# Optimization experiments

Measured on AMD Instinct MI355X. Metric: run time of the kernel, lower is better.

Reference implementation:

```python
import jax, jax.numpy as jnp
from jax import lax
import numpy as np

P, K1, K2 = 8, 5, 9  # nPaths, small/large ECA kernel sizes (from nDim=1024, nPaths=8)
LN_EPS = 1e-5


def setup_inputs() -> dict:
    key = jax.random.key(0)
    ks = jax.random.split(key, 6)
    b, c, l = 16, 1024, 4096
    return {
        "x": jax.random.normal(ks[0], (b, c, l), dtype=jnp.float32),
        "conv1_w": jax.random.normal(ks[1], (P, K1), dtype=jnp.float32) * 0.3,
        "conv2_w": jax.random.normal(ks[2], (P, K2), dtype=jnp.float32) * 0.3,
        "combine_w": jax.random.normal(ks[3], (2,), dtype=jnp.float32) * 0.5,
        "combine_b": jnp.zeros((), dtype=jnp.float32),
        "ln_g": jnp.ones((P,), dtype=jnp.float32),
        "ln_b": jnp.zeros((P,), dtype=jnp.float32),
        "W1": jax.random.normal(ks[4], (P, 2 * P), dtype=jnp.float32) * 0.3,
        "b1": jnp.zeros((2 * P,), dtype=jnp.float32),
        "W2": jax.random.normal(ks[5], (2 * P, P), dtype=jnp.float32) * 0.3,
        "b2": jnp.zeros((P,), dtype=jnp.float32),
    }


def _grouped_conv(y, w):
    # y: (b, P, D) pooled per-path features; w: (P, k) one 1-ch kernel per path.
    # Equivalent to the per-path Conv1d(1,1,k, padding=(k-1)//2) loop, fused.
    k = w.shape[-1]
    pad = (k - 1) // 2
    return lax.conv_general_dilated(
        y, w[:, None, :], window_strides=(1,), padding=[(pad, pad)],
        dimension_numbers=("NCH", "OIH", "NCH"), feature_group_count=y.shape[1])


def reference(x, conv1_w, conv2_w, combine_w, combine_b, ln_g, ln_b, W1, b1, W2, b2):
    b, c, l = x.shape
    nP = conv1_w.shape[0]
    D = c // nP
    pf = x.reshape(b, nP, D, l)          # (b, P, D, l)
    y = pf.mean(-1)                      # (b, P, D) global-avg-pool over l
    y1 = _grouped_conv(y, conv1_w)       # (b, P, D)
    y2 = _grouped_conv(y, conv2_w)       # (b, P, D)
    # combine = Conv1d(2,1,1): scalar mix of the two conv outputs + bias
    attn = jax.nn.sigmoid(combine_w[0] * y1 + combine_w[1] * y2 + combine_b)
    # cross-path gating MLP on per-path mean attention
    cross = attn.mean(-1)                # (b, P)
    mu = cross.mean(-1, keepdims=True)
    var = cross.var(-1, keepdims=True)   # biased, matches torch LayerNorm
    h = (cross - mu) / jnp.sqrt(var + LN_EPS) * ln_g + ln_b
    h = jax.nn.gelu(h @ W1 + b1, approximate=False)
    gate = jax.nn.sigmoid(h @ W2 + b2)   # (b, P)
    scale = attn * gate[:, :, None]      # (b, P, D)
    out = pf * scale[..., None]          # broadcast over l
    return out.reshape(b, c, l)
```

## Files before the change

kernel.cpp:

```cpp
#include <hip/hip_runtime.h>
#include <math.h>

#define NP 8
#define ND 128
#define NC 1024
#define NL 4096
#define NB 16
#define LN_EPS 1e-5f

#define NBLK 2048
#define NCHUNK 4
#define RPC 2
#define GRPS 64

typedef float v4f __attribute__((ext_vector_type(4)));

__device__ __forceinline__ float hsum(v4f v) { return v.x + v.y + v.z + v.w; }
__device__ __forceinline__ float sigmoid_f(float z) { return 1.f / (1.f + expf(-z)); }

__device__ __forceinline__ float gelu_f(float s) {
    const float t = 0.7978845608028654f * (s + 0.044715f * s * s * s);
    const float e = expf(2.f * t);
    return 0.5f * s * (1.f + (e - 1.f) / (e + 1.f));
}

__global__ __launch_bounds__(256, 8) void fused_kernel(
    const float* __restrict__ x, float* __restrict__ y,
    unsigned* __restrict__ garr, unsigned* __restrict__ grel,
    unsigned* __restrict__ root,
    const float* __restrict__ conv1_w, const float* __restrict__ conv2_w,
    const float* __restrict__ combine_w, const float* __restrict__ combine_b,
    const float* __restrict__ ln_g, const float* __restrict__ ln_b,
    const float* __restrict__ W1, const float* __restrict__ b1,
    const float* __restrict__ W2, const float* __restrict__ b2,
    float* __restrict__ out)
{
    const int tid    = threadIdx.x;
    const int bid    = blockIdx.x;
    const int grp    = bid >> 5;
    const bool lead  = (bid & 31) == 0;

    __shared__ float sred[RPC][4];
    __shared__ float sy[NC];
    __shared__ float sattn[NC];
    __shared__ float scross[NP];
    __shared__ float sh[NP];
    __shared__ float sh2[2 * NP];
    __shared__ float sgate[NP];
    __shared__ float sml[2];

    for (int c = 0; c < NCHUNK; ++c) {
        const int r0  = c * (NBLK * RPC) + RPC * bid;
        const int b   = r0 >> 10;
        const int ch0 = r0 & (NC - 1);
        const v4f* x0 = (const v4f*)x + (size_t)r0 * (NL / 4);
        v4f* o0       = (v4f*)out    + (size_t)r0 * (NL / 4);

        #pragma unroll
        for (int r = 0; r < RPC; ++r) {
            const v4f* xr = x0 + (size_t)r * (NL / 4);
            float ps = hsum(xr[tid]) + hsum(xr[tid + 256])
                     + hsum(xr[tid + 512]) + hsum(xr[tid + 768]);
            ps += __shfl_down(ps, 32, 64); ps += __shfl_down(ps, 16, 64);
            ps += __shfl_down(ps, 8, 64);  ps += __shfl_down(ps, 4, 64);
            ps += __shfl_down(ps, 2, 64);  ps += __shfl_down(ps, 1, 64);
            if ((tid & 63) == 0) sred[r][tid >> 6] = ps;
        }
        __syncthreads();
        if (tid == 0) {
            #pragma unroll
            for (int r = 0; r < RPC; ++r) {
                const float ym = (sred[r][0] + sred[r][1] + sred[r][2] + sred[r][3]) * (1.f / NL);
                __hip_atomic_store(&y[r0 + r], ym, __ATOMIC_RELAXED, __HIP_MEMORY_SCOPE_AGENT);
            }
            unsigned old = __hip_atomic_fetch_add(&garr[grp], 1u,
                              __ATOMIC_RELEASE, __HIP_MEMORY_SCOPE_AGENT);
            if (old == (unsigned)(c * 32 + 31))
                __hip_atomic_fetch_add(root, 1u,
                              __ATOMIC_RELEASE, __HIP_MEMORY_SCOPE_AGENT);
            if (lead) {
                while (__hip_atomic_load(root, __ATOMIC_RELAXED,
                                         __HIP_MEMORY_SCOPE_AGENT) < (unsigned)((c + 1) * GRPS))
                    __builtin_amdgcn_s_sleep(4);
                __hip_atomic_store(&grel[grp], (unsigned)(c + 1),
                                   __ATOMIC_RELAXED, __HIP_MEMORY_SCOPE_AGENT);
            } else {
                while (__hip_atomic_load(&grel[grp], __ATOMIC_RELAXED,
                                         __HIP_MEMORY_SCOPE_AGENT) < (unsigned)(c + 1))
                    __builtin_amdgcn_s_sleep(4);
            }
        }
        __syncthreads();

        const float* yb = y + b * NC;
        #pragma unroll
        for (int k = 0; k < 4; ++k) {
            const int i = tid + 256 * k;
            sy[i] = __hip_atomic_load(&yb[i], __ATOMIC_RELAXED, __HIP_MEMORY_SCOPE_AGENT);
        }
        __syncthreads();
        #pragma unroll
        for (int k = 0; k < 4; ++k) {
            const int pos = tid + 256 * k;
            const int p = pos >> 7, d = pos & 127;
            const float* rowp = sy + p * ND;
            float c1 = 0.f;
            #pragma unroll
            for (int t = 0; t < 5; ++t) {
                int dd = d + t - 2;
                float v = (dd >= 0 && dd < ND) ? rowp[dd] : 0.f;
                c1 += conv1_w[p * 5 + t] * v;
            }
            float c2 = 0.f;
            #pragma unroll
            for (int t = 0; t < 9; ++t) {
                int dd = d + t - 4;
                float v = (dd >= 0 && dd < ND) ? rowp[dd] : 0.f;
                c2 += conv2_w[p * 9 + t] * v;
            }
            sattn[pos] = sigmoid_f(combine_w[0] * c1 + combine_w[1] * c2 + combine_b[0]);
        }
        __syncthreads();
        if (tid < 128) {
            const int p = tid >> 4, o = (tid & 15) * 8;
            float s = 0.f;
            #pragma unroll
            for (int j = 0; j < 8; ++j) s += sattn[p * ND + o + j];
            s += __shfl_down(s, 8, 16); s += __shfl_down(s, 4, 16);
            s += __shfl_down(s, 2, 16); s += __shfl_down(s, 1, 16);
            if ((tid & 15) == 0) scross[p] = s * (1.f / ND);
        }
        __syncthreads();
        if (tid == 0) {
            float mu = 0.f;
            #pragma unroll
            for (int pp = 0; pp < NP; ++pp) mu += scross[pp];
            mu *= (1.f / NP);
            float var = 0.f;
            #pragma unroll
            for (int pp = 0; pp < NP; ++pp) { float dl = scross[pp] - mu; var += dl * dl; }
            sml[0] = mu;
            sml[1] = rsqrtf(var * (1.f / NP) + LN_EPS);
        }
        __syncthreads();
        if (tid < NP)
            sh[tid] = (scross[tid] - sml[0]) * sml[1] * ln_g[tid] + ln_b[tid];
        __syncthreads();
        if (tid < 2 * NP) {
            float s = b1[tid];
            #pragma unroll
            for (int pp = 0; pp < NP; ++pp) s += sh[pp] * W1[pp * (2 * NP) + tid];
            sh2[tid] = gelu_f(s);
        }
        __syncthreads();
        if (tid < NP) {
            float s = b2[tid];
            #pragma unroll
            for (int j = 0; j < 2 * NP; ++j) s += sh2[j] * W2[j * NP + tid];
            sgate[tid] = sigmoid_f(s);
        }
        __syncthreads();

        #pragma unroll
        for (int r = 0; r < RPC; ++r) {
            const float s = sattn[ch0 + r] * sgate[(ch0 + r) >> 7];
            const v4f* xr = x0 + (size_t)r * (NL / 4);
            v4f* orr      = o0 + (size_t)r * (NL / 4);
            __builtin_nontemporal_store(xr[tid]       * s, &orr[tid]);
            __builtin_nontemporal_store(xr[tid + 256] * s, &orr[tid + 256]);
            __builtin_nontemporal_store(xr[tid + 512] * s, &orr[tid + 512]);
            __builtin_nontemporal_store(xr[tid + 768] * s, &orr[tid + 768]);
        }
        __syncthreads();
    }
}

__global__ __launch_bounds__(256) void pool_kernel(const float* __restrict__ x,
                                                   float* __restrict__ y) {
    const int wid  = threadIdx.x >> 6;
    const int lane = threadIdx.x & 63;
    const int row  = blockIdx.x * 4 + wid;
    const v4f* xr = (const v4f*)(x + (size_t)row * NL);
    float s = 0.f;
    #pragma unroll
    for (int i = 0; i < 16; ++i) {
        v4f v = xr[lane + i * 64];
        s += v.x + v.y + v.z + v.w;
    }
    #pragma unroll
    for (int off = 32; off; off >>= 1) s += __shfl_down(s, off, 64);
    if (lane == 0) y[row] = s * (1.f / NL);
}

__global__ __launch_bounds__(1024) void attn_kernel(
    const float* __restrict__ y,
    const float* __restrict__ conv1_w, const float* __restrict__ conv2_w,
    const float* __restrict__ combine_w, const float* __restrict__ combine_b,
    const float* __restrict__ ln_g, const float* __restrict__ ln_b,
    const float* __restrict__ W1, const float* __restrict__ b1,
    const float* __restrict__ W2, const float* __restrict__ b2,
    float* __restrict__ scale)
{
    const int b = blockIdx.x;
    const int tid = threadIdx.x;
    const int p = tid >> 7;
    const int d = tid & 127;

    __shared__ float sy[NC];
    __shared__ float sattn[NC];
    __shared__ float sred[16];
    __shared__ float scross[NP];
    __shared__ float sh[NP];
    __shared__ float sh2[2 * NP];
    __shared__ float sgate[NP];
    __shared__ float sml[2];

    sy[tid] = y[b * NC + tid];
    __syncthreads();

    const float* rowp = sy + p * ND;
    float c1 = 0.f;
    #pragma unroll
    for (int t = 0; t < 5; ++t) {
        int dd = d + t - 2;
        float v = (dd >= 0 && dd < ND) ? rowp[dd] : 0.f;
        c1 += conv1_w[p * 5 + t] * v;
    }
    float c2 = 0.f;
    #pragma unroll
    for (int t = 0; t < 9; ++t) {
        int dd = d + t - 4;
        float v = (dd >= 0 && dd < ND) ? rowp[dd] : 0.f;
        c2 += conv2_w[p * 9 + t] * v;
    }
    const float a = sigmoid_f(combine_w[0] * c1 + combine_w[1] * c2 + combine_b[0]);
    sattn[tid] = a;

    float r = a;
    #pragma unroll
    for (int off = 32; off; off >>= 1) r += __shfl_down(r, off, 64);
    const int lane = tid & 63, wid = tid >> 6;
    if (lane == 0) sred[wid] = r;
    __syncthreads();

    if (tid == 0) {
        float mu = 0.f, var = 0.f;
        #pragma unroll
        for (int pp = 0; pp < NP; ++pp) {
            scross[pp] = (sred[2 * pp] + sred[2 * pp + 1]) * (1.f / ND);
            mu += scross[pp];
        }
        mu *= (1.f / NP);
        #pragma unroll
        for (int pp = 0; pp < NP; ++pp) { float dl = scross[pp] - mu; var += dl * dl; }
        sml[0] = mu;
        sml[1] = rsqrtf(var * (1.f / NP) + LN_EPS);
    }
    __syncthreads();
    if (tid < NP)
        sh[tid] = (scross[tid] - sml[0]) * sml[1] * ln_g[tid] + ln_b[tid];
    __syncthreads();
    if (tid < 2 * NP) {
        float s = b1[tid];
        #pragma unroll
        for (int pp = 0; pp < NP; ++pp) s += sh[pp] * W1[pp * (2 * NP) + tid];
        sh2[tid] = gelu_f(s);
    }
    __syncthreads();
    if (tid < NP) {
        float s = b2[tid];
        #pragma unroll
        for (int j = 0; j < 2 * NP; ++j) s += sh2[j] * W2[j * NP + tid];
        sgate[tid] = sigmoid_f(s);
    }
    __syncthreads();

    scale[b * NC + tid] = sattn[tid] * sgate[p];
}

__global__ __launch_bounds__(256) void scale_kernel(const float* __restrict__ x,
                                                    const float* __restrict__ scale,
                                                    float* __restrict__ out) {
    const v4f* xv = (const v4f*)x;
    v4f* ov = (v4f*)out;
    const size_t n = (size_t)NB * NC * (NL / 4);
    const size_t stride = (size_t)gridDim.x * blockDim.x;
    for (size_t i = (size_t)blockIdx.x * blockDim.x + threadIdx.x; i < n; i += stride) {
        const float s = scale[i >> 10];
        v4f v = xv[i];
        v *= s;
        __builtin_nontemporal_store(v, &ov[i]);
    }
}

extern "C" void kernel_launch(void* const* d_in, const int* in_sizes, int n_in,
                              void* d_out, int out_size, void* d_ws, size_t ws_size,
                              hipStream_t stream) {
    const float* x         = (const float*)d_in[0];
    const float* conv1_w   = (const float*)d_in[1];
    const float* conv2_w   = (const float*)d_in[2];
    const float* combine_w = (const float*)d_in[3];
    const float* combine_b = (const float*)d_in[4];
    const float* ln_g      = (const float*)d_in[5];
    const float* ln_b      = (const float*)d_in[6];
    const float* W1        = (const float*)d_in[7];
    const float* b1        = (const float*)d_in[8];
    const float* W2        = (const float*)d_in[9];
    const float* b2        = (const float*)d_in[10];
    float* out = (float*)d_out;

    float* y        = (float*)d_ws;
    float* scale    = y + NB * NC;
    unsigned* garr  = (unsigned*)(void*)scale;
    unsigned* grel  = garr + GRPS;
    unsigned* root  = grel + GRPS;

    hipMemsetAsync((void*)garr, 0, (2 * GRPS + 16) * sizeof(unsigned), stream);

    int nb = 0;
    hipOccupancyMaxActiveBlocksPerMultiprocessor(&nb, fused_kernel, 256, 0);
    if (nb >= NBLK / 256) {
        void* args[] = { (void*)&x, (void*)&y, (void*)&garr, (void*)&grel, (void*)&root,
                         (void*)&conv1_w, (void*)&conv2_w,
                         (void*)&combine_w, (void*)&combine_b,
                         (void*)&ln_g, (void*)&ln_b,
                         (void*)&W1, (void*)&b1, (void*)&W2, (void*)&b2,
                         (void*)&out };
        hipLaunchCooperativeKernel((const void*)fused_kernel, dim3(NBLK), dim3(256),
                                   args, 0, stream);
    } else {
        pool_kernel<<<NB * NC / 4, 256, 0, stream>>>(x, y);
        attn_kernel<<<NB, 1024, 0, stream>>>(y, conv1_w, conv2_w, combine_w, combine_b,
                                             ln_g, ln_b, W1, b1, W2, b2, scale);
        scale_kernel<<<2048, 256, 0, stream>>>(x, scale, out);
    }
}
```

Before: 137.3 us.

## Stage input rows in LDS to avoid re-reading x after grid barrier

Each block now copies its two rows of x into shared memory during the pooling pass and scales them from LDS after the grid-wide sync, instead of reading x from global memory a second time. To do this, blocks grow to 512 threads (one 256-thread half per row), the grid shrinks to 1024 blocks, and the chunk count doubles to 8. The attention computation is reorganised so each thread keeps its two attention values in registers and reduces them with one wave shuffle, which removes the sattn array. The cost is about 32KB of LDS per block, which limits residency, and twice as many grid-wide barrier rounds.

```diff
diff --git a/kernel.cpp b/kernel.cpp
--- a/kernel.cpp
+++ b/kernel.cpp
@@ -8,10 +8,11 @@
 #define NB 16
 #define LN_EPS 1e-5f
 
-#define NBLK 2048
-#define NCHUNK 4
-#define RPC 2
-#define GRPS 64
+#define NBLK 1024
+#define NT   512
+#define RPC  2
+#define NCHUNK 8
+#define GRPS 32
 
 typedef float v4f __attribute__((ext_vector_type(4)));
 
@@ -24,7 +25,7 @@
     return 0.5f * s * (1.f + (e - 1.f) / (e + 1.f));
 }
 
-__global__ __launch_bounds__(256, 8) void fused_kernel(
+__global__ __launch_bounds__(NT, 8) void fused_kernel(
     const float* __restrict__ x, float* __restrict__ y,
     unsigned* __restrict__ garr, unsigned* __restrict__ grel,
     unsigned* __restrict__ root,
@@ -35,43 +36,47 @@
     const float* __restrict__ W2, const float* __restrict__ b2,
     float* __restrict__ out)
 {
-    const int tid    = threadIdx.x;
-    const int bid    = blockIdx.x;
-    const int grp    = bid >> 5;
-    const bool lead  = (bid & 31) == 0;
-
+    const int tid  = threadIdx.x;
+    const int bid  = blockIdx.x;
+    const int grp  = bid >> 5;
+    const bool lead = (bid & 31) == 0;
+    const int r    = tid >> 8;
+    const int col  = tid & 255;
+
+    __shared__ v4f   srow[RPC][NL / 4];
+    __shared__ float sy[NC];
     __shared__ float sred[RPC][4];
-    __shared__ float sy[NC];
-    __shared__ float sattn[NC];
     __shared__ float scross[NP];
     __shared__ float sh[NP];
     __shared__ float sh2[2 * NP];
     __shared__ float sgate[NP];
     __shared__ float sml[2];
+    __shared__ float sscale[RPC];
 
     for (int c = 0; c < NCHUNK; ++c) {
         const int r0  = c * (NBLK * RPC) + RPC * bid;
         const int b   = r0 >> 10;
         const int ch0 = r0 & (NC - 1);
-        const v4f* x0 = (const v4f*)x + (size_t)r0 * (NL / 4);
-        v4f* o0       = (v4f*)out    + (size_t)r0 * (NL / 4);
-
-        #pragma unroll
-        for (int r = 0; r < RPC; ++r) {
-            const v4f* xr = x0 + (size_t)r * (NL / 4);
-            float ps = hsum(xr[tid]) + hsum(xr[tid + 256])
-                     + hsum(xr[tid + 512]) + hsum(xr[tid + 768]);
+
+        {
+            const v4f* xr = (const v4f*)x + (size_t)(r0 + r) * (NL / 4);
+            v4f v0 = xr[col], v1 = xr[col + 256], v2 = xr[col + 512], v3 = xr[col + 768];
+            srow[r][col]       = v0;
+            srow[r][col + 256] = v1;
+            srow[r][col + 512] = v2;
+            srow[r][col + 768] = v3;
+            float ps = hsum(v0) + hsum(v1) + hsum(v2) + hsum(v3);
             ps += __shfl_down(ps, 32, 64); ps += __shfl_down(ps, 16, 64);
             ps += __shfl_down(ps, 8, 64);  ps += __shfl_down(ps, 4, 64);
             ps += __shfl_down(ps, 2, 64);  ps += __shfl_down(ps, 1, 64);
-            if ((tid & 63) == 0) sred[r][tid >> 6] = ps;
+            if ((tid & 63) == 0) sred[r][(tid >> 6) & 3] = ps;
         }
         __syncthreads();
         if (tid == 0) {
             #pragma unroll
-            for (int r = 0; r < RPC; ++r) {
-                const float ym = (sred[r][0] + sred[r][1] + sred[r][2] + sred[r][3]) * (1.f / NL);
-                __hip_atomic_store(&y[r0 + r], ym, __ATOMIC_RELAXED, __HIP_MEMORY_SCOPE_AGENT);
+            for (int rr = 0; rr < RPC; ++rr) {
+                const float ym = (sred[rr][0] + sred[rr][1] + sred[rr][2] + sred[rr][3]) * (1.f / NL);
+                __hip_atomic_store(&y[r0 + rr], ym, __ATOMIC_RELAXED, __HIP_MEMORY_SCOPE_AGENT);
             }
             unsigned old = __hip_atomic_fetch_add(&garr[grp], 1u,
                               __ATOMIC_RELEASE, __HIP_MEMORY_SCOPE_AGENT);
@@ -92,43 +97,41 @@
         }
         __syncthreads();
 
-        const float* yb = y + b * NC;
-        #pragma unroll
-        for (int k = 0; k < 4; ++k) {
-            const int i = tid + 256 * k;
-            sy[i] = __hip_atomic_load(&yb[i], __ATOMIC_RELAXED, __HIP_MEMORY_SCOPE_AGENT);
-        }
-        __syncthreads();
-        #pragma unroll
-        for (int k = 0; k < 4; ++k) {
-            const int pos = tid + 256 * k;
-            const int p = pos >> 7, d = pos & 127;
-            const float* rowp = sy + p * ND;
-            float c1 = 0.f;
-            #pragma unroll
-            for (int t = 0; t < 5; ++t) {
-                int dd = d + t - 2;
-                float v = (dd >= 0 && dd < ND) ? rowp[dd] : 0.f;
-                c1 += conv1_w[p * 5 + t] * v;
+        {
+            const float* yb = y + b * NC;
+            sy[tid]       = __hip_atomic_load(&yb[tid],       __ATOMIC_RELAXED, __HIP_MEMORY_SCOPE_AGENT);
+            sy[tid + 512] = __hip_atomic_load(&yb[tid + 512], __ATOMIC_RELAXED, __HIP_MEMORY_SCOPE_AGENT);
+        }
+        __syncthreads();
+        float aa0, aa1;
+        {
+            #pragma unroll
+            for (int k = 0; k < 2; ++k) {
+                const int pos = 2 * tid + k;
+                const int p = pos >> 7, d = pos & 127;
+                const float* rowp = sy + p * ND;
+                float c1 = 0.f;
+                #pragma unroll
+                for (int t = 0; t < 5; ++t) {
+                    int dd = d + t - 2;
+                    float v = (dd >= 0 && dd < ND) ? rowp[dd] : 0.f;
+                    c1 += conv1_w[p * 5 + t] * v;
+                }
+                float c2 = 0.f;
+                #pragma unroll
+                for (int t = 0; t < 9; ++t) {
+                    int dd = d + t - 4;
+                    float v = (dd >= 0 && dd < ND) ? rowp[dd] : 0.f;
+                    c2 += conv2_w[p * 9 + t] * v;
+                }
+                const float a = sigmoid_f(combine_w[0] * c1 + combine_w[1] * c2 + combine_b[0]);
+                if (k == 0) aa0 = a; else aa1 = a;
             }
-            float c2 = 0.f;
-            #pragma unroll
-            for (int t = 0; t < 9; ++t) {
-                int dd = d + t - 4;
-                float v = (dd >= 0 && dd < ND) ? rowp[dd] : 0.f;
-                c2 += conv2_w[p * 9 + t] * v;
-            }
-            sattn[pos] = sigmoid_f(combine_w[0] * c1 + combine_w[1] * c2 + combine_b[0]);
-        }
-        __syncthreads();
-        if (tid < 128) {
-            const int p = tid >> 4, o = (tid & 15) * 8;
-            float s = 0.f;
-            #pragma unroll
-            for (int j = 0; j < 8; ++j) s += sattn[p * ND + o + j];
-            s += __shfl_down(s, 8, 16); s += __shfl_down(s, 4, 16);
-            s += __shfl_down(s, 2, 16); s += __shfl_down(s, 1, 16);
-            if ((tid & 15) == 0) scross[p] = s * (1.f / ND);
+            float s = aa0 + aa1;
+            s += __shfl_down(s, 32, 64); s += __shfl_down(s, 16, 64);
+            s += __shfl_down(s, 8, 64);  s += __shfl_down(s, 4, 64);
+            s += __shfl_down(s, 2, 64);  s += __shfl_down(s, 1, 64);
+            if ((tid & 63) == 0) scross[tid >> 6] = s * (1.f / ND);
         }
         __syncthreads();
         if (tid == 0) {
@@ -160,16 +163,20 @@
             sgate[tid] = sigmoid_f(s);
         }
         __syncthreads();
-
-        #pragma unroll
-        for (int r = 0; r < RPC; ++r) {
-            const float s = sattn[ch0 + r] * sgate[(ch0 + r) >> 7];
-            const v4f* xr = x0 + (size_t)r * (NL / 4);
-            v4f* orr      = o0 + (size_t)r * (NL / 4);
-            __builtin_nontemporal_store(xr[tid]       * s, &orr[tid]);
-            __builtin_nontemporal_store(xr[tid + 256] * s, &orr[tid + 256]);
-            __builtin_nontemporal_store(xr[tid + 512] * s, &orr[tid + 512]);
-            __builtin_nontemporal_store(xr[tid + 768] * s, &orr[tid + 768]);
+        if (tid == (ch0 >> 1)) {
+            const float g = sgate[ch0 >> 7];
+            sscale[0] = aa0 * g;
+            sscale[1] = aa1 * g;
+        }
+        __syncthreads();
+
+        {
+            const float sc = sscale[r];
+            v4f* orow = (v4f*)out + (size_t)(r0 + r) * (NL / 4);
+            __builtin_nontemporal_store(srow[r][col]       * sc, &orow[col]);
+            __builtin_nontemporal_store(srow[r][col + 256] * sc, &orow[col + 256]);
+            __builtin_nontemporal_store(srow[r][col + 512] * sc, &orow[col + 512]);
+            __builtin_nontemporal_store(srow[r][col + 768] * sc, &orow[col + 768]);
         }
         __syncthreads();
     }
@@ -236,11 +243,11 @@
     const float a = sigmoid_f(combine_w[0] * c1 + combine_w[1] * c2 + combine_b[0]);
     sattn[tid] = a;
 
-    float r = a;
-    #pragma unroll
-    for (int off = 32; off; off >>= 1) r += __shfl_down(r, off, 64);
+    float rr = a;
+    #pragma unroll
+    for (int off = 32; off; off >>= 1) rr += __shfl_down(rr, off, 64);
     const int lane = tid & 63, wid = tid >> 6;
-    if (lane == 0) sred[wid] = r;
+    if (lane == 0) sred[wid] = rr;
     __syncthreads();
 
     if (tid == 0) {
@@ -318,15 +325,15 @@
     hipMemsetAsync((void*)garr, 0, (2 * GRPS + 16) * sizeof(unsigned), stream);
 
     int nb = 0;
-    hipOccupancyMaxActiveBlocksPerMultiprocessor(&nb, fused_kernel, 256, 0);
-    if (nb >= NBLK / 256) {
+    hipOccupancyMaxActiveBlocksPerMultiprocessor(&nb, fused_kernel, NT, 0);
+    if (nb >= 4) {
         void* args[] = { (void*)&x, (void*)&y, (void*)&garr, (void*)&grel, (void*)&root,
                          (void*)&conv1_w, (void*)&conv2_w,
                          (void*)&combine_w, (void*)&combine_b,
                          (void*)&ln_g, (void*)&ln_b,
                          (void*)&W1, (void*)&b1, (void*)&W2, (void*)&b2,
                          (void*)&out };
-        hipLaunchCooperativeKernel((const void*)fused_kernel, dim3(NBLK), dim3(256),
+        hipLaunchCooperativeKernel((const void*)fused_kernel, dim3(NBLK), dim3(NT),
                                    args, 0, stream);
     } else {
         pool_kernel<<<NB * NC / 4, 256, 0, stream>>>(x, y);
```

New measurement: 137.3 us. Within noise of the previous version (-0.1%).
